# Kernel optimization log

Measured on AMD Instinct MI355X. Metric: run time of the kernel, lower is better.

The kernel has to match this reference:

```python
import jax, jax.numpy as jnp
import numpy as np

B, T, D, E, I = 8, 8192, 128, 8, 16
EPS = 1e-5


def setup_inputs() -> dict:
    key = jax.random.key(0)
    ks = jax.random.split(key, 6)
    return {
        "x": jax.random.normal(ks[0], (B, T, D), dtype=jnp.float32),
        "ln_g": jnp.ones((D,), dtype=jnp.float32),
        "ln_b": jnp.zeros((D,), dtype=jnp.float32),
        "gate_w": jax.random.normal(ks[1], (D, E), dtype=jnp.float32) * (1.0 / np.sqrt(D)),
        "gate_b": jnp.zeros((E,), dtype=jnp.float32),
        "w1": jax.random.normal(ks[2], (E, D, I), dtype=jnp.float32),
        "w2": jax.random.normal(ks[3], (E, I, D), dtype=jnp.float32),
    }


def reference(x, ln_g, ln_b, gate_w, gate_b, w1, w2):
    # LayerNorm (torch default eps=1e-5)
    mu = jnp.mean(x, axis=-1, keepdims=True)
    var = jnp.mean(jnp.square(x - mu), axis=-1, keepdims=True)
    x_norm = (x - mu) * jax.lax.rsqrt(var + EPS) * ln_g + ln_b

    # Dense gating + softmax routing
    gating_logits = x_norm @ gate_w + gate_b          # [B,T,E]
    routing_weights = jax.nn.softmax(gating_logits, axis=-1)

    # All-expert FFN: small batched GEMMs (torch F.gelu default = exact erf)
    y = jax.nn.gelu(jnp.einsum('btc,eci->btei', x_norm, w1), approximate=False)
    moe_experts_out = jnp.einsum('btei,eic->btec', y, w2)  # [B,T,E,D]
    moe_agg = jnp.einsum('btec,bte->btc', moe_experts_out, routing_weights)

    return (x + moe_agg, gating_logits, moe_experts_out)
```

## Files before the change

### kernel.cpp

```cpp
#include <hip/hip_runtime.h>
#include <math.h>

#define O1_OFF 8388608
#define O2_OFF 8912896

typedef __attribute__((ext_vector_type(8))) short short8;
typedef __attribute__((ext_vector_type(4))) float f32x4;

static __device__ __forceinline__ unsigned short f2bf(float f) {
    unsigned u = __builtin_bit_cast(unsigned, f);
    u = (u + 0x7fffu + ((u >> 16) & 1u)) >> 16;
    return (unsigned short)u;
}

static __device__ __forceinline__ int swz(int row, int chunk) {
    return row * 256 + ((chunk ^ (row & 7)) << 4);
}

static __device__ __forceinline__ int tswz(int row, int col) {
    int chunk = (col >> 3) ^ ((row >> 1) & 6);
    return row * 256 + (chunk << 4) + ((col & 7) << 1);
}

static __device__ __forceinline__ void bar_lds() {
    asm volatile("s_waitcnt lgkmcnt(0)" ::: "memory");
    __builtin_amdgcn_s_barrier();
    asm volatile("" ::: "memory");
}

static __device__ __forceinline__ void fence_lds() {
    asm volatile("s_waitcnt lgkmcnt(0)" ::: "memory");
}

__global__ __launch_bounds__(256, 2) void moe_fused(
    const float* __restrict__ x, const float* __restrict__ ln_g,
    const float* __restrict__ ln_b, const float* __restrict__ gate_w,
    const float* __restrict__ gate_b, const float* __restrict__ w1,
    const float* __restrict__ w2, float* __restrict__ out)
{
    __shared__ __align__(16) char smem[67584];
    char* pXY = smem;
    char* pW  = smem + 16384;
    char* pTR = smem + 49152;
    float* pRW = (float*)(smem + 65536);

    const int t = threadIdx.x;
    const int l = t & 63;
    const int w = t >> 6;
    const int tok0 = blockIdx.x * 64;

    const int colq = (t & 31) * 4;
    const int rsub = t >> 5;

    const int rb = w * 16;
    const int col = l & 15;
    const int ak = l >> 4;
    const int arow = rb + col;

    float4 xv[8];
    {
        const float* xb = x + (size_t)tok0 * 128;
        #pragma unroll
        for (int s = 0; s < 8; ++s)
            xv[s] = *(const float4*)(xb + s * 1024 + t * 4);
    }
    float4 g4 = *(const float4*)(ln_g + colq);
    float4 b4 = *(const float4*)(ln_b + colq);

    const int e2 = t >> 5;
    unsigned pk[4][8];
    {
        #pragma unroll
        for (int cc = 0; cc < 4; ++cc)
            #pragma unroll
            for (int q = 0; q < 8; ++q) pk[cc][q] = 0u;
        const float* w2b = w2 + e2 * 2048 + colq;
        #pragma unroll
        for (int i = 0; i < 16; ++i) {
            float4 q4 = *(const float4*)(w2b + i * 128);
            unsigned sh = (i & 1) * 16;
            pk[0][i >> 1] |= (unsigned)f2bf(q4.x) << sh;
            pk[1][i >> 1] |= (unsigned)f2bf(q4.y) << sh;
            pk[2][i >> 1] |= (unsigned)f2bf(q4.z) << sh;
            pk[3][i >> 1] |= (unsigned)f2bf(q4.w) << sh;
        }
    }

    {
        const int p = t & 127, ch = t >> 7;
        const float* w1b = w1 + (p >> 4) * 2048 + (p & 15);
        #pragma unroll
        for (int cc = 0; cc < 8; ++cc) {
            short8 v;
            #pragma unroll
            for (int j = 0; j < 8; ++j)
                v[j] = (short)f2bf(w1b[(ch * 64 + cc * 8 + j) * 16]);
            *(short8*)(pW + swz(p, ch * 8 + cc)) = v;
        }
    }

    short8 gfr[4];
    float4 gb4;
    {
        #pragma unroll
        for (int ks = 0; ks < 4; ++ks)
            #pragma unroll
            for (int j = 0; j < 8; ++j) {
                float v = (col < 8) ? gate_w[(32 * ks + 8 * ak + j) * 8 + col] : 0.0f;
                gfr[ks][j] = (short)f2bf(v);
            }
        gb4 = *(const float4*)(gate_b + (ak & 1) * 4);
    }

    #pragma unroll
    for (int s = 0; s < 8; ++s) {
        float4 v = xv[s];
        float sm = v.x + v.y + v.z + v.w;
        float sq = v.x*v.x + v.y*v.y + v.z*v.z + v.w*v.w;
        #pragma unroll
        for (int m = 1; m < 32; m <<= 1) {
            sm += __shfl_xor(sm, m, 64);
            sq += __shfl_xor(sq, m, 64);
        }
        float mu = sm * (1.0f / 128.0f);
        float var = sq * (1.0f / 128.0f) - mu * mu;
        float rs = rsqrtf(var + 1e-5f);
        float n0 = (v.x - mu) * rs * g4.x + b4.x;
        float n1 = (v.y - mu) * rs * g4.y + b4.y;
        float n2 = (v.z - mu) * rs * g4.z + b4.z;
        float n3 = (v.w - mu) * rs * g4.w + b4.w;
        unsigned lo = (unsigned)f2bf(n0) | ((unsigned)f2bf(n1) << 16);
        unsigned hi = (unsigned)f2bf(n2) | ((unsigned)f2bf(n3) << 16);
        unsigned long long dvv = (unsigned long long)lo | ((unsigned long long)hi << 32);
        int row = s * 8 + rsub;
        *(unsigned long long*)(pXY + swz(row, colq >> 3) + (colq & 7) * 2) = dvv;
    }

    bar_lds();

    const f32x4 zero4 = {0.f, 0.f, 0.f, 0.f};
    const short8 zfrag = {0, 0, 0, 0, 0, 0, 0, 0};

    short8 afr[4];
    #pragma unroll
    for (int ks = 0; ks < 4; ++ks)
        afr[ks] = *(const short8*)(pXY + swz(arow, ks * 4 + ak));

    f32x4 accg = zero4;
    #pragma unroll
    for (int ks = 0; ks < 4; ++ks)
        accg = __builtin_amdgcn_mfma_f32_16x16x32_bf16(gfr[ks], afr[ks], accg, 0, 0, 0);

    const size_t trow = (size_t)(tok0 + arow);
    {
        float lg0 = accg[0] + gb4.x;
        float lg1 = accg[1] + gb4.y;
        float lg2 = accg[2] + gb4.z;
        float lg3 = accg[3] + gb4.w;
        if (ak < 2) {
            f32x4 lgv = {lg0, lg1, lg2, lg3};
            *(f32x4*)(out + O1_OFF + trow * 8 + ak * 4) = lgv;
        }
        float mx = fmaxf(fmaxf(lg0, lg1), fmaxf(lg2, lg3));
        mx = fmaxf(mx, __shfl_xor(mx, 16, 64));
        float ex0 = __expf(lg0 - mx), ex1 = __expf(lg1 - mx);
        float ex2 = __expf(lg2 - mx), ex3 = __expf(lg3 - mx);
        float sm = ex0 + ex1 + ex2 + ex3;
        sm += __shfl_xor(sm, 16, 64);
        float inv = 1.0f / sm;
        if (ak < 2) {
            f32x4 pv = {ex0 * inv, ex1 * inv, ex2 * inv, ex3 * inv};
            *(f32x4*)(pRW + arow * 8 + ak * 4) = pv;
        }
    }

    f32x4 accb[8];
    #pragma unroll
    for (int nt = 0; nt < 8; ++nt) accb[nt] = zero4;
    #pragma unroll
    for (int ks = 0; ks < 4; ++ks)
        #pragma unroll
        for (int nt = 0; nt < 8; ++nt) {
            short8 wfr = *(const short8*)(pW + swz(nt * 16 + col, ks * 4 + ak));
            accb[nt] = __builtin_amdgcn_mfma_f32_16x16x32_bf16(wfr, afr[ks], accb[nt], 0, 0, 0);
        }

    #pragma unroll
    for (int nt = 0; nt < 8; ++nt) {
        float y0 = accb[nt][0], y1 = accb[nt][1], y2 = accb[nt][2], y3 = accb[nt][3];
        y0 = 0.5f * y0 * (1.0f + erff(y0 * 0.70710678118654752f));
        y1 = 0.5f * y1 * (1.0f + erff(y1 * 0.70710678118654752f));
        y2 = 0.5f * y2 * (1.0f + erff(y2 * 0.70710678118654752f));
        y3 = 0.5f * y3 * (1.0f + erff(y3 * 0.70710678118654752f));
        unsigned lo = (unsigned)f2bf(y0) | ((unsigned)f2bf(y1) << 16);
        unsigned hi = (unsigned)f2bf(y2) | ((unsigned)f2bf(y3) << 16);
        unsigned long long dv = (unsigned long long)lo | ((unsigned long long)hi << 32);
        *(unsigned long long*)(pXY + swz(arow, nt * 2 + (ak >> 1)) + (ak & 1) * 8) = dv;
    }

    bar_lds();

    #pragma unroll
    for (int cc = 0; cc < 4; ++cc) {
        int c = colq + cc;
        int rc = e2 * 128 + c;
        int a = (c >> 2) & 3;
        *(uint4*)(pW + (((rc * 2 + 0) ^ a) << 4)) =
            make_uint4(pk[cc][0], pk[cc][1], pk[cc][2], pk[cc][3]);
        *(uint4*)(pW + (((rc * 2 + 1) ^ a) << 4)) =
            make_uint4(pk[cc][4], pk[cc][5], pk[cc][6], pk[cc][7]);
    }

    bar_lds();

    f32x4 agg[8];
    #pragma unroll
    for (int nt = 0; nt < 8; ++nt) agg[nt] = zero4;

    #pragma unroll
    for (int e = 0; e < 8; ++e) {
        float rwe[4];
        #pragma unroll
        for (int r = 0; r < 4; ++r)
            rwe[r] = pRW[(rb + ak * 4 + r) * 8 + e];
        short8 alo = *(const short8*)(pXY + swz(arow, 2 * e + (ak & 1)));
        short8 af = (ak < 2) ? alo : zfrag;
        f32x4 ot[8];
        #pragma unroll
        for (int nt = 0; nt < 8; ++nt) {
            int c = nt * 16 + col;
            int rc = e * 128 + c;
            int a = (c >> 2) & 3;
            short8 blo = *(const short8*)(pW + (((rc * 2 + (ak & 1)) ^ a) << 4));
            short8 bf = (ak < 2) ? blo : zfrag;
            ot[nt] = __builtin_amdgcn_mfma_f32_16x16x32_bf16(af, bf, zero4, 0, 0, 0);
            #pragma unroll
            for (int r = 0; r < 4; ++r)
                agg[nt][r] += rwe[r] * ot[nt][r];
        }
        #pragma unroll
        for (int nt = 0; nt < 8; ++nt)
            #pragma unroll
            for (int r = 0; r < 4; ++r)
                *(unsigned short*)(pTR + tswz(rb + ak * 4 + r, nt * 16 + col)) = f2bf(ot[nt][r]);
        fence_lds();
        #pragma unroll
        for (int i2 = 0; i2 < 8; ++i2) {
            int row = rb + i2 * 2 + (l >> 5);
            int c0 = (l & 31) * 4;
            unsigned long long raw = *(const unsigned long long*)(pTR + tswz(row, c0));
            unsigned lo = (unsigned)raw, hi = (unsigned)(raw >> 32);
            f32x4 v;
            v[0] = __builtin_bit_cast(float, lo << 16);
            v[1] = __builtin_bit_cast(float, lo & 0xffff0000u);
            v[2] = __builtin_bit_cast(float, hi << 16);
            v[3] = __builtin_bit_cast(float, hi & 0xffff0000u);
            *(f32x4*)(out + O2_OFF + (size_t)(tok0 + row) * 1024 + e * 128 + c0) = v;
        }
        asm volatile("" ::: "memory");
    }

    bar_lds();

    #pragma unroll
    for (int nt = 0; nt < 8; ++nt) {
        int c = nt * 16 + col;
        #pragma unroll
        for (int r = 0; r < 4; ++r) {
            int row = rb + ak * 4 + r;
            *(float*)(pW + row * 512 + ((c << 2) ^ ((row & 4) << 2))) = agg[nt][r];
        }
    }

    bar_lds();

    #pragma unroll
    for (int s = 0; s < 8; ++s) {
        int row = s * 8 + rsub;
        f32x4 a4 = *(const f32x4*)(pW + row * 512 + ((colq << 2) ^ ((row & 4) << 2)));
        float4 o;
        o.x = xv[s].x + a4[0];
        o.y = xv[s].y + a4[1];
        o.z = xv[s].z + a4[2];
        o.w = xv[s].w + a4[3];
        *(float4*)(out + (size_t)(tok0 + row) * 128 + colq) = o;
    }
}

extern "C" void kernel_launch(void* const* d_in, const int* in_sizes, int n_in,
                              void* d_out, int out_size, void* d_ws, size_t ws_size,
                              hipStream_t stream) {
    const float* x      = (const float*)d_in[0];
    const float* ln_g   = (const float*)d_in[1];
    const float* ln_b   = (const float*)d_in[2];
    const float* gate_w = (const float*)d_in[3];
    const float* gate_b = (const float*)d_in[4];
    const float* w1     = (const float*)d_in[5];
    const float* w2     = (const float*)d_in[6];
    float* out = (float*)d_out;
    (void)in_sizes; (void)n_in; (void)out_size; (void)d_ws; (void)ws_size;
    moe_fused<<<dim3(1024), dim3(256), 0, stream>>>(x, ln_g, ln_b, gate_w, gate_b, w1, w2, out);
}
```

Measured before the change: 80.89 us.

## Process two 64-token tiles per block and prefetch the second tile's inputs

Result: slower. 163.8 us (+102.4%).

```diff
diff --git a/kernel.cpp b/kernel.cpp
--- a/kernel.cpp
+++ b/kernel.cpp
@@ -47,7 +47,8 @@
     const int t = threadIdx.x;
     const int l = t & 63;
     const int w = t >> 6;
-    const int tok0 = blockIdx.x * 64;
+    const int tok0a = blockIdx.x * 128;
+    const int tok0b = tok0a + 64;
 
     const int colq = (t & 31) * 4;
     const int rsub = t >> 5;
@@ -56,37 +57,25 @@
     const int col = l & 15;
     const int ak = l >> 4;
     const int arow = rb + col;
-
-    float4 xv[8];
-    {
+    const int e2 = t >> 5;
+
+    const f32x4 zero4 = {0.f, 0.f, 0.f, 0.f};
+    const short8 zfrag = {0, 0, 0, 0, 0, 0, 0, 0};
+
+    float4 xv1[8], xv2[8];
+    unsigned pk[4][8];
+    short8 wbuf[8];
+    short8 gfr[4];
+    float4 g4, b4, gb4;
+
+    auto load_x = [&](float4 xv[8], int tok0) {
         const float* xb = x + (size_t)tok0 * 128;
         #pragma unroll
         for (int s = 0; s < 8; ++s)
             xv[s] = *(const float4*)(xb + s * 1024 + t * 4);
-    }
-    float4 g4 = *(const float4*)(ln_g + colq);
-    float4 b4 = *(const float4*)(ln_b + colq);
-
-    const int e2 = t >> 5;
-    unsigned pk[4][8];
-    {
-        #pragma unroll
-        for (int cc = 0; cc < 4; ++cc)
-            #pragma unroll
-            for (int q = 0; q < 8; ++q) pk[cc][q] = 0u;
-        const float* w2b = w2 + e2 * 2048 + colq;
-        #pragma unroll
-        for (int i = 0; i < 16; ++i) {
-            float4 q4 = *(const float4*)(w2b + i * 128);
-            unsigned sh = (i & 1) * 16;
-            pk[0][i >> 1] |= (unsigned)f2bf(q4.x) << sh;
-            pk[1][i >> 1] |= (unsigned)f2bf(q4.y) << sh;
-            pk[2][i >> 1] |= (unsigned)f2bf(q4.z) << sh;
-            pk[3][i >> 1] |= (unsigned)f2bf(q4.w) << sh;
-        }
-    }
-
-    {
+    };
+
+    auto w1_loads = [&]() {
         const int p = t & 127, ch = t >> 7;
         const float* w1b = w1 + (p >> 4) * 2048 + (p & 15);
         #pragma unroll
@@ -95,64 +84,51 @@
             #pragma unroll
             for (int j = 0; j < 8; ++j)
                 v[j] = (short)f2bf(w1b[(ch * 64 + cc * 8 + j) * 16]);
-            *(short8*)(pW + swz(p, ch * 8 + cc)) = v;
-        }
-    }
-
-    short8 gfr[4];
-    float4 gb4;
-    {
+            wbuf[cc] = v;
+        }
+    };
+    auto w1_writes = [&]() {
+        const int p = t & 127, ch = t >> 7;
+        #pragma unroll
+        for (int cc = 0; cc < 8; ++cc)
+            *(short8*)(pW + swz(p, ch * 8 + cc)) = wbuf[cc];
+    };
+
+    auto ln_to_lds = [&](const float4 xv[8]) {
+        #pragma unroll
+        for (int s = 0; s < 8; ++s) {
+            float4 v = xv[s];
+            float sm = v.x + v.y + v.z + v.w;
+            float sq = v.x*v.x + v.y*v.y + v.z*v.z + v.w*v.w;
+            #pragma unroll
+            for (int m = 1; m < 32; m <<= 1) {
+                sm += __shfl_xor(sm, m, 64);
+                sq += __shfl_xor(sq, m, 64);
+            }
+            float mu = sm * (1.0f / 128.0f);
+            float var = sq * (1.0f / 128.0f) - mu * mu;
+            float rs = rsqrtf(var + 1e-5f);
+            float n0 = (v.x - mu) * rs * g4.x + b4.x;
+            float n1 = (v.y - mu) * rs * g4.y + b4.y;
+            float n2 = (v.z - mu) * rs * g4.z + b4.z;
+            float n3 = (v.w - mu) * rs * g4.w + b4.w;
+            unsigned lo = (unsigned)f2bf(n0) | ((unsigned)f2bf(n1) << 16);
+            unsigned hi = (unsigned)f2bf(n2) | ((unsigned)f2bf(n3) << 16);
+            unsigned long long dvv = (unsigned long long)lo | ((unsigned long long)hi << 32);
+            int row = s * 8 + rsub;
+            *(unsigned long long*)(pXY + swz(row, colq >> 3) + (colq & 7) * 2) = dvv;
+        }
+    };
+
+    auto gating = [&](short8 afr[4], int tok0) {
         #pragma unroll
         for (int ks = 0; ks < 4; ++ks)
-            #pragma unroll
-            for (int j = 0; j < 8; ++j) {
-                float v = (col < 8) ? gate_w[(32 * ks + 8 * ak + j) * 8 + col] : 0.0f;
-                gfr[ks][j] = (short)f2bf(v);
-            }
-        gb4 = *(const float4*)(gate_b + (ak & 1) * 4);
-    }
-
-    #pragma unroll
-    for (int s = 0; s < 8; ++s) {
-        float4 v = xv[s];
-        float sm = v.x + v.y + v.z + v.w;
-        float sq = v.x*v.x + v.y*v.y + v.z*v.z + v.w*v.w;
-        #pragma unroll
-        for (int m = 1; m < 32; m <<= 1) {
-            sm += __shfl_xor(sm, m, 64);
-            sq += __shfl_xor(sq, m, 64);
-        }
-        float mu = sm * (1.0f / 128.0f);
-        float var = sq * (1.0f / 128.0f) - mu * mu;
-        float rs = rsqrtf(var + 1e-5f);
-        float n0 = (v.x - mu) * rs * g4.x + b4.x;
-        float n1 = (v.y - mu) * rs * g4.y + b4.y;
-        float n2 = (v.z - mu) * rs * g4.z + b4.z;
-        float n3 = (v.w - mu) * rs * g4.w + b4.w;
-        unsigned lo = (unsigned)f2bf(n0) | ((unsigned)f2bf(n1) << 16);
-        unsigned hi = (unsigned)f2bf(n2) | ((unsigned)f2bf(n3) << 16);
-        unsigned long long dvv = (unsigned long long)lo | ((unsigned long long)hi << 32);
-        int row = s * 8 + rsub;
-        *(unsigned long long*)(pXY + swz(row, colq >> 3) + (colq & 7) * 2) = dvv;
-    }
-
-    bar_lds();
-
-    const f32x4 zero4 = {0.f, 0.f, 0.f, 0.f};
-    const short8 zfrag = {0, 0, 0, 0, 0, 0, 0, 0};
-
-    short8 afr[4];
-    #pragma unroll
-    for (int ks = 0; ks < 4; ++ks)
-        afr[ks] = *(const short8*)(pXY + swz(arow, ks * 4 + ak));
-
-    f32x4 accg = zero4;
-    #pragma unroll
-    for (int ks = 0; ks < 4; ++ks)
-        accg = __builtin_amdgcn_mfma_f32_16x16x32_bf16(gfr[ks], afr[ks], accg, 0, 0, 0);
-
-    const size_t trow = (size_t)(tok0 + arow);
-    {
+            afr[ks] = *(const short8*)(pXY + swz(arow, ks * 4 + ak));
+        f32x4 accg = zero4;
+        #pragma unroll
+        for (int ks = 0; ks < 4; ++ks)
+            accg = __builtin_amdgcn_mfma_f32_16x16x32_bf16(gfr[ks], afr[ks], accg, 0, 0, 0);
+        const size_t trow = (size_t)(tok0 + arow);
         float lg0 = accg[0] + gb4.x;
         float lg1 = accg[1] + gb4.y;
         float lg2 = accg[2] + gb4.z;
@@ -172,119 +148,196 @@
             f32x4 pv = {ex0 * inv, ex1 * inv, ex2 * inv, ex3 * inv};
             *(f32x4*)(pRW + arow * 8 + ak * 4) = pv;
         }
-    }
-
-    f32x4 accb[8];
-    #pragma unroll
-    for (int nt = 0; nt < 8; ++nt) accb[nt] = zero4;
-    #pragma unroll
-    for (int ks = 0; ks < 4; ++ks)
+    };
+
+    auto stageB_gelu = [&](const short8 afr[4]) {
+        f32x4 accb[8];
+        #pragma unroll
+        for (int nt = 0; nt < 8; ++nt) accb[nt] = zero4;
+        #pragma unroll
+        for (int ks = 0; ks < 4; ++ks)
+            #pragma unroll
+            for (int nt = 0; nt < 8; ++nt) {
+                short8 wfr = *(const short8*)(pW + swz(nt * 16 + col, ks * 4 + ak));
+                accb[nt] = __builtin_amdgcn_mfma_f32_16x16x32_bf16(wfr, afr[ks], accb[nt], 0, 0, 0);
+            }
         #pragma unroll
         for (int nt = 0; nt < 8; ++nt) {
-            short8 wfr = *(const short8*)(pW + swz(nt * 16 + col, ks * 4 + ak));
-            accb[nt] = __builtin_amdgcn_mfma_f32_16x16x32_bf16(wfr, afr[ks], accb[nt], 0, 0, 0);
-        }
-
-    #pragma unroll
-    for (int nt = 0; nt < 8; ++nt) {
-        float y0 = accb[nt][0], y1 = accb[nt][1], y2 = accb[nt][2], y3 = accb[nt][3];
-        y0 = 0.5f * y0 * (1.0f + erff(y0 * 0.70710678118654752f));
-        y1 = 0.5f * y1 * (1.0f + erff(y1 * 0.70710678118654752f));
-        y2 = 0.5f * y2 * (1.0f + erff(y2 * 0.70710678118654752f));
-        y3 = 0.5f * y3 * (1.0f + erff(y3 * 0.70710678118654752f));
-        unsigned lo = (unsigned)f2bf(y0) | ((unsigned)f2bf(y1) << 16);
-        unsigned hi = (unsigned)f2bf(y2) | ((unsigned)f2bf(y3) << 16);
-        unsigned long long dv = (unsigned long long)lo | ((unsigned long long)hi << 32);
-        *(unsigned long long*)(pXY + swz(arow, nt * 2 + (ak >> 1)) + (ak & 1) * 8) = dv;
-    }
-
-    bar_lds();
-
-    #pragma unroll
-    for (int cc = 0; cc < 4; ++cc) {
-        int c = colq + cc;
-        int rc = e2 * 128 + c;
-        int a = (c >> 2) & 3;
-        *(uint4*)(pW + (((rc * 2 + 0) ^ a) << 4)) =
-            make_uint4(pk[cc][0], pk[cc][1], pk[cc][2], pk[cc][3]);
-        *(uint4*)(pW + (((rc * 2 + 1) ^ a) << 4)) =
-            make_uint4(pk[cc][4], pk[cc][5], pk[cc][6], pk[cc][7]);
-    }
-
-    bar_lds();
-
-    f32x4 agg[8];
-    #pragma unroll
-    for (int nt = 0; nt < 8; ++nt) agg[nt] = zero4;
-
-    #pragma unroll
-    for (int e = 0; e < 8; ++e) {
-        float rwe[4];
-        #pragma unroll
-        for (int r = 0; r < 4; ++r)
-            rwe[r] = pRW[(rb + ak * 4 + r) * 8 + e];
-        short8 alo = *(const short8*)(pXY + swz(arow, 2 * e + (ak & 1)));
-        short8 af = (ak < 2) ? alo : zfrag;
-        f32x4 ot[8];
+            float y0 = accb[nt][0], y1 = accb[nt][1], y2 = accb[nt][2], y3 = accb[nt][3];
+            y0 = 0.5f * y0 * (1.0f + erff(y0 * 0.70710678118654752f));
+            y1 = 0.5f * y1 * (1.0f + erff(y1 * 0.70710678118654752f));
+            y2 = 0.5f * y2 * (1.0f + erff(y2 * 0.70710678118654752f));
+            y3 = 0.5f * y3 * (1.0f + erff(y3 * 0.70710678118654752f));
+            unsigned lo = (unsigned)f2bf(y0) | ((unsigned)f2bf(y1) << 16);
+            unsigned hi = (unsigned)f2bf(y2) | ((unsigned)f2bf(y3) << 16);
+            unsigned long long dv = (unsigned long long)lo | ((unsigned long long)hi << 32);
+            *(unsigned long long*)(pXY + swz(arow, nt * 2 + (ak >> 1)) + (ak & 1) * 8) = dv;
+        }
+    };
+
+    auto w2t_write = [&]() {
+        #pragma unroll
+        for (int cc = 0; cc < 4; ++cc) {
+            int c = colq + cc;
+            int rc = e2 * 128 + c;
+            int a = (c >> 2) & 3;
+            *(uint4*)(pW + (((rc * 2 + 0) ^ a) << 4)) =
+                make_uint4(pk[cc][0], pk[cc][1], pk[cc][2], pk[cc][3]);
+            *(uint4*)(pW + (((rc * 2 + 1) ^ a) << 4)) =
+                make_uint4(pk[cc][4], pk[cc][5], pk[cc][6], pk[cc][7]);
+        }
+    };
+
+    auto p4 = [&](f32x4 agg[8], int tok0, bool pref) {
+        #pragma unroll
+        for (int nt = 0; nt < 8; ++nt) agg[nt] = zero4;
+        #pragma unroll
+        for (int e = 0; e < 8; ++e) {
+            if (pref && e == 5)
+                load_x(xv2, tok0 + 64);
+            float rwe[4];
+            #pragma unroll
+            for (int r = 0; r < 4; ++r)
+                rwe[r] = pRW[(rb + ak * 4 + r) * 8 + e];
+            short8 alo = *(const short8*)(pXY + swz(arow, 2 * e + (ak & 1)));
+            short8 af = (ak < 2) ? alo : zfrag;
+            f32x4 ot[8];
+            #pragma unroll
+            for (int nt = 0; nt < 8; ++nt) {
+                int c = nt * 16 + col;
+                int rc = e * 128 + c;
+                int a = (c >> 2) & 3;
+                short8 blo = *(const short8*)(pW + (((rc * 2 + (ak & 1)) ^ a) << 4));
+                short8 bf = (ak < 2) ? blo : zfrag;
+                ot[nt] = __builtin_amdgcn_mfma_f32_16x16x32_bf16(af, bf, zero4, 0, 0, 0);
+                #pragma unroll
+                for (int r = 0; r < 4; ++r)
+                    agg[nt][r] += rwe[r] * ot[nt][r];
+            }
+            #pragma unroll
+            for (int nt = 0; nt < 8; ++nt)
+                #pragma unroll
+                for (int r = 0; r < 4; ++r)
+                    *(unsigned short*)(pTR + tswz(rb + ak * 4 + r, nt * 16 + col)) = f2bf(ot[nt][r]);
+            fence_lds();
+            #pragma unroll
+            for (int i2 = 0; i2 < 8; ++i2) {
+                int row = rb + i2 * 2 + (l >> 5);
+                int c0 = (l & 31) * 4;
+                unsigned long long raw = *(const unsigned long long*)(pTR + tswz(row, c0));
+                unsigned lo = (unsigned)raw, hi = (unsigned)(raw >> 32);
+                f32x4 v;
+                v[0] = __builtin_bit_cast(float, lo << 16);
+                v[1] = __builtin_bit_cast(float, lo & 0xffff0000u);
+                v[2] = __builtin_bit_cast(float, hi << 16);
+                v[3] = __builtin_bit_cast(float, hi & 0xffff0000u);
+                *(f32x4*)(out + O2_OFF + (size_t)(tok0 + row) * 1024 + e * 128 + c0) = v;
+            }
+            asm volatile("" ::: "memory");
+        }
+    };
+
+    auto epi_agg_write = [&](const f32x4 agg[8]) {
         #pragma unroll
         for (int nt = 0; nt < 8; ++nt) {
             int c = nt * 16 + col;
-            int rc = e * 128 + c;
-            int a = (c >> 2) & 3;
-            short8 blo = *(const short8*)(pW + (((rc * 2 + (ak & 1)) ^ a) << 4));
-            short8 bf = (ak < 2) ? blo : zfrag;
-            ot[nt] = __builtin_amdgcn_mfma_f32_16x16x32_bf16(af, bf, zero4, 0, 0, 0);
-            #pragma unroll
-            for (int r = 0; r < 4; ++r)
-                agg[nt][r] += rwe[r] * ot[nt][r];
-        }
-        #pragma unroll
-        for (int nt = 0; nt < 8; ++nt)
-            #pragma unroll
-            for (int r = 0; r < 4; ++r)
-                *(unsigned short*)(pTR + tswz(rb + ak * 4 + r, nt * 16 + col)) = f2bf(ot[nt][r]);
-        fence_lds();
-        #pragma unroll
-        for (int i2 = 0; i2 < 8; ++i2) {
-            int row = rb + i2 * 2 + (l >> 5);
-            int c0 = (l & 31) * 4;
-            unsigned long long raw = *(const unsigned long long*)(pTR + tswz(row, c0));
-            unsigned lo = (unsigned)raw, hi = (unsigned)(raw >> 32);
-            f32x4 v;
-            v[0] = __builtin_bit_cast(float, lo << 16);
-            v[1] = __builtin_bit_cast(float, lo & 0xffff0000u);
-            v[2] = __builtin_bit_cast(float, hi << 16);
-            v[3] = __builtin_bit_cast(float, hi & 0xffff0000u);
-            *(f32x4*)(out + O2_OFF + (size_t)(tok0 + row) * 1024 + e * 128 + c0) = v;
-        }
-        asm volatile("" ::: "memory");
+            #pragma unroll
+            for (int r = 0; r < 4; ++r) {
+                int row = rb + ak * 4 + r;
+                *(float*)(pW + row * 512 + ((c << 2) ^ ((row & 4) << 2))) = agg[nt][r];
+            }
+        }
+    };
+
+    auto epi_read_store = [&](const float4 xv[8], int tok0) {
+        #pragma unroll
+        for (int s = 0; s < 8; ++s) {
+            int row = s * 8 + rsub;
+            f32x4 a4 = *(const f32x4*)(pW + row * 512 + ((colq << 2) ^ ((row & 4) << 2)));
+            float4 o;
+            o.x = xv[s].x + a4[0];
+            o.y = xv[s].y + a4[1];
+            o.z = xv[s].z + a4[2];
+            o.w = xv[s].w + a4[3];
+            *(float4*)(out + (size_t)(tok0 + row) * 128 + colq) = o;
+        }
+    };
+
+    load_x(xv1, tok0a);
+    g4 = *(const float4*)(ln_g + colq);
+    b4 = *(const float4*)(ln_b + colq);
+
+    {
+        #pragma unroll
+        for (int cc = 0; cc < 4; ++cc)
+            #pragma unroll
+            for (int q = 0; q < 8; ++q) pk[cc][q] = 0u;
+        const float* w2b = w2 + e2 * 2048 + colq;
+        #pragma unroll
+        for (int i = 0; i < 16; ++i) {
+            float4 q4 = *(const float4*)(w2b + i * 128);
+            unsigned sh = (i & 1) * 16;
+            pk[0][i >> 1] |= (unsigned)f2bf(q4.x) << sh;
+            pk[1][i >> 1] |= (unsigned)f2bf(q4.y) << sh;
+            pk[2][i >> 1] |= (unsigned)f2bf(q4.z) << sh;
+            pk[3][i >> 1] |= (unsigned)f2bf(q4.w) << sh;
+        }
     }
 
-    bar_lds();
-
-    #pragma unroll
-    for (int nt = 0; nt < 8; ++nt) {
-        int c = nt * 16 + col;
-        #pragma unroll
-        for (int r = 0; r < 4; ++r) {
-            int row = rb + ak * 4 + r;
-            *(float*)(pW + row * 512 + ((c << 2) ^ ((row & 4) << 2))) = agg[nt][r];
-        }
+    w1_loads();
+    w1_writes();
+
+    {
+        #pragma unroll
+        for (int ks = 0; ks < 4; ++ks)
+            #pragma unroll
+            for (int j = 0; j < 8; ++j) {
+                float v = (col < 8) ? gate_w[(32 * ks + 8 * ak + j) * 8 + col] : 0.0f;
+                gfr[ks][j] = (short)f2bf(v);
+            }
+        gb4 = *(const float4*)(gate_b + (ak & 1) * 4);
     }
 
-    bar_lds();
-
-    #pragma unroll
-    for (int s = 0; s < 8; ++s) {
-        int row = s * 8 + rsub;
-        f32x4 a4 = *(const f32x4*)(pW + row * 512 + ((colq << 2) ^ ((row & 4) << 2)));
-        float4 o;
-        o.x = xv[s].x + a4[0];
-        o.y = xv[s].y + a4[1];
-        o.z = xv[s].z + a4[2];
-        o.w = xv[s].w + a4[3];
-        *(float4*)(out + (size_t)(tok0 + row) * 128 + colq) = o;
-    }
+    ln_to_lds(xv1);
+    bar_lds();
+
+    short8 afr[4];
+    gating(afr, tok0a);
+    stageB_gelu(afr);
+    bar_lds();
+
+    w2t_write();
+    bar_lds();
+
+    f32x4 agg[8];
+    p4(agg, tok0a, true);
+    bar_lds();
+
+    epi_agg_write(agg);
+    ln_to_lds(xv2);
+    bar_lds();
+
+    w1_loads();
+    epi_read_store(xv1, tok0a);
+    gating(afr, tok0b);
+    bar_lds();
+
+    w1_writes();
+    bar_lds();
+
+    stageB_gelu(afr);
+    bar_lds();
+
+    w2t_write();
+    bar_lds();
+
+    p4(agg, tok0b, false);
+    bar_lds();
+
+    epi_agg_write(agg);
+    bar_lds();
+
+    epi_read_store(xv2, tok0b);
 }
 
 extern "C" void kernel_launch(void* const* d_in, const int* in_sizes, int n_in,
@@ -299,5 +352,5 @@
     const float* w2     = (const float*)d_in[6];
     float* out = (float*)d_out;
     (void)in_sizes; (void)n_in; (void)out_size; (void)d_ws; (void)ws_size;
-    moe_fused<<<dim3(1024), dim3(256), 0, stream>>>(x, ln_g, ln_b, gate_w, gate_b, w1, w2, out);
-}
+    moe_fused<<<dim3(512), dim3(256), 0, stream>>>(x, ln_g, ln_b, gate_w, gate_b, w1, w2, out);
+}
```
